# Optimization experiments

Measured on AMD Instinct MI355X. Metric: run time of the kernel, lower is better.

Reference implementation:

```python
import jax, jax.numpy as jnp
import numpy as np
import math

B, C_IN, H, W_DIM, D_DIM = 2, 128, 24, 24, 24
D_MODEL, N_HEAD, N_LAYERS, D_FF = 256, 8, 4, 512
D_K = D_MODEL // N_HEAD
EPS = 1e-6


def setup_inputs() -> dict:
    key = jax.random.key(0)
    ks = jax.random.split(key, 16)
    s = 0.02
    inp = {
        "x": jax.random.normal(ks[0], (B, C_IN, H, W_DIM, D_DIM), jnp.float32),
        # 1x1x1 Conv3d W_x: weight [out, in], bias [out]
        "Wx_w": jax.random.normal(ks[1], (D_MODEL, C_IN), jnp.float32) * s,
        "Wx_b": jnp.zeros((D_MODEL,), jnp.float32),
        # per-layer attention projections (stacked over layers)
        "Wq": jax.random.normal(ks[2], (N_LAYERS, D_MODEL, D_MODEL), jnp.float32) * s,
        "bq": jnp.zeros((N_LAYERS, D_MODEL), jnp.float32),
        "Wk": jax.random.normal(ks[3], (N_LAYERS, D_MODEL, D_MODEL), jnp.float32) * s,
        "bk": jnp.zeros((N_LAYERS, D_MODEL), jnp.float32),
        "Wv": jax.random.normal(ks[4], (N_LAYERS, D_MODEL, D_MODEL), jnp.float32) * s,
        "bv": jnp.zeros((N_LAYERS, D_MODEL), jnp.float32),
        "Wo": jax.random.normal(ks[5], (N_LAYERS, D_MODEL, D_MODEL), jnp.float32) * s,
        "bo": jnp.zeros((N_LAYERS, D_MODEL), jnp.float32),
        # layer norms
        "ln1_g": jnp.ones((N_LAYERS, D_MODEL), jnp.float32),
        "ln1_b": jnp.zeros((N_LAYERS, D_MODEL), jnp.float32),
        "ln2_g": jnp.ones((N_LAYERS, D_MODEL), jnp.float32),
        "ln2_b": jnp.zeros((N_LAYERS, D_MODEL), jnp.float32),
        # FFN
        "ffn_w1": jax.random.normal(ks[6], (N_LAYERS, D_MODEL, D_FF), jnp.float32) * s,
        "ffn_b1": jnp.zeros((N_LAYERS, D_FF), jnp.float32),
        "ffn_w2": jax.random.normal(ks[7], (N_LAYERS, D_FF, D_MODEL), jnp.float32) * s,
        "ffn_b2": jnp.zeros((N_LAYERS, D_MODEL), jnp.float32),
        # depthwise 3x3x3 conv positional encoder (groups = D_MODEL)
        "pos_w": jax.random.normal(ks[8], (N_LAYERS, D_MODEL, 1, 3, 3, 3), jnp.float32) * s,
        "pos_b": jnp.zeros((N_LAYERS, D_MODEL), jnp.float32),
    }
    return inp


def _layer_norm(t, g, b):
    mu = jnp.mean(t, axis=-1, keepdims=True)
    var = jnp.var(t, axis=-1, keepdims=True)
    return (t - mu) * jax.lax.rsqrt(var + EPS) * g + b


def reference(x, Wx_w, Wx_b, Wq, bq, Wk, bk, Wv, bv, Wo, bo,
              ln1_g, ln1_b, ln2_g, ln2_b,
              ffn_w1, ffn_b1, ffn_w2, ffn_b2, pos_w, pos_b):
    b = x.shape[0]
    # 1x1x1 conv projection W_x + ReLU (is_up=False path)
    x = jnp.einsum('bchwd,oc->bohwd', x, Wx_w) + Wx_b[None, :, None, None, None]
    x = jax.nn.relu(x)

    inv_sqrt_dk = 1.0 / math.sqrt(D_K)

    for i in range(N_LAYERS):
        # flatten spatial -> tokens: [b, n, d_model]
        t = jnp.transpose(x.reshape(b, D_MODEL, -1), (0, 2, 1))
        n = t.shape[1]

        def heads(y):  # [b,n,d] -> [b,h,n,dk]
            return jnp.transpose(y.reshape(b, n, N_HEAD, D_K), (0, 2, 1, 3))

        q = heads(t @ Wq[i] + bq[i])
        k = heads(t @ Wk[i] + bk[i])
        v = heads(t @ Wv[i] + bv[i])

        # linear attention: softmax over feature dim for q, token dim for k
        q = jax.nn.softmax(q, axis=-1) * inv_sqrt_dk
        k = jax.nn.softmax(k, axis=-2)
        ctx = jnp.einsum('bhnd,bhne->bhde', k, v)     # [b,h,dk,dk]
        o = jnp.einsum('bhnd,bhde->bhne', q, ctx)      # [b,h,n,dk]
        o = jnp.transpose(o, (0, 2, 1, 3)).reshape(b, n, D_MODEL)
        o = o @ Wo[i] + bo[i]

        t = _layer_norm(t + o, ln1_g[i], ln1_b[i])
        f = jax.nn.gelu(t @ ffn_w1[i] + ffn_b1[i], approximate=False) @ ffn_w2[i] + ffn_b2[i]
        t = _layer_norm(t + f, ln2_g[i], ln2_b[i])

        # back to volume and depthwise conv positional embedding
        x = jnp.transpose(t, (0, 2, 1)).reshape(b, D_MODEL, H, W_DIM, D_DIM)
        pos = jax.lax.conv_general_dilated(
            x, pos_w[i], window_strides=(1, 1, 1), padding='SAME',
            dimension_numbers=('NCDHW', 'OIDHW', 'NCDHW'),
            feature_group_count=D_MODEL,
        ) + pos_b[i][None, :, None, None, None]
        x = x + pos
    return x
```

## Files before the change

kernel.cpp:

```cpp
#include <hip/hip_runtime.h>
#include <math.h>

#define NTOK 13824
#define MTOT 27648
#define BATCH 2
#define CIN 128
#define DMODEL 256
#define NHEAD 8
#define NLAYERS 4
#define DFF 512
#define NSPLIT 27
#define KVHALF ((size_t)BATCH * 256 * NTOK)

typedef float f32x4 __attribute__((ext_vector_type(4)));
typedef __bf16 bf16x8 __attribute__((ext_vector_type(8)));
typedef __attribute__((address_space(1))) void gvoid;
typedef __attribute__((address_space(3))) void lvoid;

#define GLDS16(g, l) __builtin_amdgcn_global_load_lds((gvoid*)(g), (lvoid*)(l), 16, 0, 0)

__device__ __forceinline__ unsigned short f2bf(float f) {
    unsigned u = __float_as_uint(f);
    return (unsigned short)((u + 0x7FFFu + ((u >> 16) & 1u)) >> 16);
}
__device__ __forceinline__ float bf2f(unsigned short h) {
    return __uint_as_float(((unsigned)h) << 16);
}

template<int ACT, int OUTM>
__global__ __launch_bounds__(256) void gemm_bf16(
    const unsigned short* __restrict__ A, int lda,
    const unsigned short* __restrict__ Bt, int ldb,
    const float* __restrict__ bias,
    float* __restrict__ Cf, unsigned short* __restrict__ Cb,
    int ldc, int K, long sA, long sB, long sC)
{
    A  += (size_t)blockIdx.z * sA;
    Bt += (size_t)blockIdx.z * sB;
    if (OUTM == 2) Cf += (size_t)blockIdx.z * sC;
    Cb += (size_t)blockIdx.z * sC;

    __shared__ __attribute__((aligned(16))) unsigned short As[4096];
    __shared__ __attribute__((aligned(16))) unsigned short Bs[4096];
    const int t    = threadIdx.x;
    const int lane = t & 63;
    const int wave = t >> 6;
    const int wm = wave & 1, wn = wave >> 1;
    const int m0 = blockIdx.x * 128, n0 = blockIdx.y * 128;

    const int r0   = t >> 2;
    const int koff = (t & 3) * 8;
    const unsigned short* ga0 = A  + (size_t)(m0 + r0)      * lda + koff;
    const unsigned short* ga1 = A  + (size_t)(m0 + r0 + 64) * lda + koff;
    const unsigned short* gb0 = Bt + (size_t)(n0 + r0)      * ldb + koff;
    const unsigned short* gb1 = Bt + (size_t)(n0 + r0 + 64) * ldb + koff;
    unsigned short* la0 = As + t * 8;
    unsigned short* la1 = As + t * 8 + 2048;
    unsigned short* lb0 = Bs + t * 8;
    unsigned short* lb1 = Bs + t * 8 + 2048;

    f32x4 acc[4][4];
    #pragma unroll
    for (int i = 0; i < 4; ++i)
        #pragma unroll
        for (int j = 0; j < 4; ++j) acc[i][j] = (f32x4)0.0f;

    const int fm = lane & 15;
    const int fq = (lane >> 4) * 8;
    const int arow = (wm * 64 + fm) * 32 + fq;
    const int brow = (wn * 64 + fm) * 32 + fq;

    for (int k0 = 0; k0 < K; k0 += 32) {
        GLDS16(ga0 + k0, la0);
        GLDS16(ga1 + k0, la1);
        GLDS16(gb0 + k0, lb0);
        GLDS16(gb1 + k0, lb1);
        __syncthreads();
        bf16x8 af[4], bg[4];
        #pragma unroll
        for (int i = 0; i < 4; ++i) af[i] = *(const bf16x8*)(As + arow + i * 512);
        #pragma unroll
        for (int j = 0; j < 4; ++j) bg[j] = *(const bf16x8*)(Bs + brow + j * 512);
        #pragma unroll
        for (int i = 0; i < 4; ++i)
            #pragma unroll
            for (int j = 0; j < 4; ++j)
                acc[i][j] = __builtin_amdgcn_mfma_f32_16x16x32_bf16(
                    af[i], bg[j], acc[i][j], 0, 0, 0);
        __syncthreads();
    }

    const int cb  = n0 + wn * 64 + fm;
    const int rbs = m0 + wm * 64 + (lane >> 4) * 4;
    #pragma unroll
    for (int j = 0; j < 4; ++j) {
        const int n = cb + j * 16;
        const float bv = bias[n];
        #pragma unroll
        for (int i = 0; i < 4; ++i) {
            #pragma unroll
            for (int r = 0; r < 4; ++r) {
                float v = acc[i][j][r] + bv;
                if (ACT == 1) v = fmaxf(v, 0.0f);
                if (ACT == 2) v = 0.5f * v * (1.0f + erff(v * 0.7071067811865476f));
                const size_t off = (size_t)(rbs + i * 16 + r) * ldc + n;
                if (OUTM == 2) Cf[off] = v;
                Cb[off] = f2bf(v);
            }
        }
    }
}

#define CW_QKV  786432
#define CW_O   1048576
#define CW_1   1572864
#define CW_2   2097152
#define CW_X   2129920
#define CW_B   2132992
__global__ __launch_bounds__(256) void conv_weights(
    const float* __restrict__ Wq, const float* __restrict__ Wk,
    const float* __restrict__ Wv, const float* __restrict__ Wo,
    const float* __restrict__ fw1, const float* __restrict__ fw2,
    const float* __restrict__ Wx_w,
    const float* __restrict__ bq, const float* __restrict__ bk,
    const float* __restrict__ bv,
    unsigned short* __restrict__ wqkv_t, unsigned short* __restrict__ wo_t,
    unsigned short* __restrict__ w1_t, unsigned short* __restrict__ w2_t,
    unsigned short* __restrict__ wx_bf, float* __restrict__ bqkv)
{
    const int e = blockIdx.x * 256 + threadIdx.x;
    if (e < CW_QKV) {
        const int i = e / 196608, r = e % 196608;
        const int n = r / 256, k = r % 256;
        const float* src = (n < 256) ? Wq : (n < 512) ? Wk : Wv;
        wqkv_t[e] = f2bf(src[((size_t)i * 256 + k) * 256 + (n & 255)]);
    } else if (e < CW_O) {
        const int r = e - CW_QKV;
        const int i = r / 65536, rr = r % 65536, n = rr / 256, k = rr % 256;
        wo_t[r] = f2bf(Wo[((size_t)i * 256 + k) * 256 + n]);
    } else if (e < CW_1) {
        const int r = e - CW_O;
        const int i = r / 131072, rr = r % 131072, n = rr / 256, k = rr % 256;
        w1_t[r] = f2bf(fw1[((size_t)i * 256 + k) * 512 + n]);
    } else if (e < CW_2) {
        const int r = e - CW_1;
        const int i = r / 131072, rr = r % 131072, n = rr / 512, k = rr % 512;
        w2_t[r] = f2bf(fw2[((size_t)i * 512 + k) * 256 + n]);
    } else if (e < CW_X) {
        const int r = e - CW_2;
        wx_bf[r] = f2bf(Wx_w[r]);
    } else if (e < CW_B) {
        const int r = e - CW_X;
        const int i = r / 768, j = r % 768;
        const float v = (j < 256) ? bq[i * 256 + j]
                      : (j < 512) ? bk[i * 256 + j - 256]
                                  : bv[i * 256 + j - 512];
        bqkv[r] = v;
    }
}

__global__ __launch_bounds__(256) void conv_x(
    const float* __restrict__ x, unsigned short* __restrict__ xbf)
{
    __shared__ float tile[32][33];
    const int n0 = blockIdx.x * 32;
    const int c0 = blockIdx.y * 32;
    const int b  = blockIdx.z;
    const int t = threadIdx.x;
    const int tn = t & 31, tc = t >> 5;
    #pragma unroll
    for (int p = 0; p < 4; ++p)
        tile[tc + p * 8][tn] =
            x[((size_t)(b * CIN + c0 + tc + p * 8)) * NTOK + n0 + tn];
    __syncthreads();
    const int cc = t & 31, nr = t >> 5;
    #pragma unroll
    for (int p = 0; p < 4; ++p)
        xbf[((size_t)(b * NTOK + n0 + nr + p * 8)) * CIN + c0 + cc] =
            f2bf(tile[cc][nr + p * 8]);
}

__global__ __launch_bounds__(256) void qsm_kernel(unsigned short* __restrict__ qkv)
{
    const int g = blockIdx.x * 256 + threadIdx.x;
    const int row = g >> 5;
    const int cg  = g & 31;
    unsigned short* p = qkv + (size_t)row * 768 + cg * 8;
    uint4 raw = *(const uint4*)p;
    unsigned short* rp = (unsigned short*)&raw;
    float v[8];
    #pragma unroll
    for (int j = 0; j < 8; ++j) v[j] = bf2f(rp[j]);
    float m = v[0];
    #pragma unroll
    for (int j = 1; j < 8; ++j) m = fmaxf(m, v[j]);
    m = fmaxf(m, __shfl_xor(m, 1, 64));
    m = fmaxf(m, __shfl_xor(m, 2, 64));
    float s = 0.0f;
    #pragma unroll
    for (int j = 0; j < 8; ++j) { v[j] = __expf(v[j] - m); s += v[j]; }
    s += __shfl_xor(s, 1, 64);
    s += __shfl_xor(s, 2, 64);
    const float r = 1.0f / s;
    #pragma unroll
    for (int j = 0; j < 8; ++j) rp[j] = f2bf(v[j] * r);
    *(uint4*)p = raw;
}

__global__ __launch_bounds__(256) void kvt_kernel(
    const unsigned short* __restrict__ qkv, unsigned short* __restrict__ kvT)
{
    const int nb = blockIdx.x, h = blockIdx.y, b = blockIdx.z;
    const int n0 = nb * 64;
    const int t = threadIdx.x;
    __shared__ __attribute__((aligned(16))) unsigned short LT[64 * 72];
    const int tl = t >> 2, cg = t & 3;
    const unsigned short* src =
        qkv + ((size_t)(b * NTOK + n0 + tl)) * 768 + 256 + h * 32 + cg * 8;
    const uint4 kr = *(const uint4*)src;
    const uint4 vr = *(const uint4*)(src + 256);
    const unsigned short* ks = (const unsigned short*)&kr;
    const unsigned short* vs = (const unsigned short*)&vr;
    #pragma unroll
    for (int j = 0; j < 8; ++j) {
        const int ch = cg * 8 + j;
        LT[ch * 72 + tl]        = f2bf(__expf(bf2f(ks[j])));
        LT[(32 + ch) * 72 + tl] = vs[j];
    }
    __syncthreads();
    #pragma unroll
    for (int it = 0; it < 2; ++it) {
        const int idx = it * 256 + t;
        const int row = idx >> 3, seg = idx & 7;
        const uint4 val = *(const uint4*)(LT + row * 72 + seg * 8);
        const int ch = row & 31;
        const size_t dst = ((row >= 32) ? KVHALF : (size_t)0)
                         + ((size_t)(b * 256 + h * 32 + ch)) * NTOK + n0 + seg * 8;
        *(uint4*)(kvT + dst) = val;
    }
}

__global__ __launch_bounds__(256) void ctx_mfma(
    const unsigned short* __restrict__ kvT,
    float* __restrict__ ctxp, float* __restrict__ skp)
{
    const int s = blockIdx.x, h = blockIdx.y, b = blockIdx.z;
    const int t = threadIdx.x, w = t >> 6, l = t & 63;
    const int fm = l & 15, fq = (l >> 4) * 8;
    const size_t rowA = (size_t)(b * 256 + h * 32 + fm) * NTOK;
    const int n0 = s * 512 + w * 128 + fq;
    const unsigned short* pa = kvT + rowA + n0;
    const unsigned short* pb = kvT + KVHALF + rowA + n0;

    f32x4 acc[2][2];
    #pragma unroll
    for (int x = 0; x < 2; ++x)
        #pragma unroll
        for (int y = 0; y < 2; ++y) acc[x][y] = (f32x4)0.0f;
    float ss0 = 0.0f, ss1 = 0.0f;

    #pragma unroll
    for (int step = 0; step < 4; ++step) {
        const int ko = step * 32;
        const uint4 ra0 = *(const uint4*)(pa + ko);
        const uint4 ra1 = *(const uint4*)(pa + (size_t)16 * NTOK + ko);
        const uint4 rb0 = *(const uint4*)(pb + ko);
        const uint4 rb1 = *(const uint4*)(pb + (size_t)16 * NTOK + ko);
        const bf16x8 a0 = *(const bf16x8*)&ra0;
        const bf16x8 a1 = *(const bf16x8*)&ra1;
        const bf16x8 b0 = *(const bf16x8*)&rb0;
        const bf16x8 b1 = *(const bf16x8*)&rb1;
        acc[0][0] = __builtin_amdgcn_mfma_f32_16x16x32_bf16(a0, b0, acc[0][0], 0, 0, 0);
        acc[0][1] = __builtin_amdgcn_mfma_f32_16x16x32_bf16(a0, b1, acc[0][1], 0, 0, 0);
        acc[1][0] = __builtin_amdgcn_mfma_f32_16x16x32_bf16(a1, b0, acc[1][0], 0, 0, 0);
        acc[1][1] = __builtin_amdgcn_mfma_f32_16x16x32_bf16(a1, b1, acc[1][1], 0, 0, 0);
        const unsigned short* u0 = (const unsigned short*)&ra0;
        const unsigned short* u1 = (const unsigned short*)&ra1;
        #pragma unroll
        for (int j = 0; j < 8; ++j) { ss0 += bf2f(u0[j]); ss1 += bf2f(u1[j]); }
    }

    ss0 += __shfl_xor(ss0, 16, 64); ss0 += __shfl_xor(ss0, 32, 64);
    ss1 += __shfl_xor(ss1, 16, 64); ss1 += __shfl_xor(ss1, 32, 64);
    __shared__ float skw[4][32];
    __shared__ float redc[4][32][33];
    if (l < 16) { skw[w][fm] = ss0; skw[w][16 + fm] = ss1; }

    const int rb4 = (l >> 4) * 4;
    #pragma unroll
    for (int x = 0; x < 2; ++x)
        #pragma unroll
        for (int y = 0; y < 2; ++y)
            #pragma unroll
            for (int r = 0; r < 4; ++r)
                redc[w][x * 16 + rb4 + r][y * 16 + fm] = acc[x][y][r];
    __syncthreads();

    if (t < 32)
        skp[(size_t)s * 512 + b * 256 + h * 32 + t] =
            skw[0][t] + skw[1][t] + skw[2][t] + skw[3][t];

    const int e0 = t * 4;
    const int dd = e0 >> 5, c0 = e0 & 31;
    float4 o;
    o.x = redc[0][dd][c0+0] + redc[1][dd][c0+0] + redc[2][dd][c0+0] + redc[3][dd][c0+0];
    o.y = redc[0][dd][c0+1] + redc[1][dd][c0+1] + redc[2][dd][c0+1] + redc[3][dd][c0+1];
    o.z = redc[0][dd][c0+2] + redc[1][dd][c0+2] + redc[2][dd][c0+2] + redc[3][dd][c0+2];
    o.w = redc[0][dd][c0+3] + redc[1][dd][c0+3] + redc[2][dd][c0+3] + redc[3][dd][c0+3];
    *(float4*)(ctxp + ((size_t)s * 16 + b * 8 + h) * 1024 + e0) = o;
}

__global__ __launch_bounds__(256) void ctxred(
    const float* __restrict__ ctxp, const float* __restrict__ skp,
    float* __restrict__ ctx, float* __restrict__ Sk)
{
    const int o = blockIdx.x * 256 + threadIdx.x;
    if (o < 16384) {
        float a = 0.0f;
        for (int s = 0; s < NSPLIT; ++s) a += ctxp[(size_t)s * 16384 + o];
        ctx[o] = a;
    } else {
        const int c = o - 16384;
        float a = 0.0f;
        for (int s = 0; s < NSPLIT; ++s) a += skp[(size_t)s * 512 + c];
        Sk[c] = a;
    }
}

__global__ __launch_bounds__(256) void ctxwo_kernel(
    const float* __restrict__ ctx, const float* __restrict__ Sk,
    const unsigned short* __restrict__ wo_t, unsigned short* __restrict__ wp)
{
    const int h = blockIdx.x, b = blockIdx.y;
    const int n = threadIdx.x;
    __shared__ float cl[1024];
    __shared__ float sdk[32];
    {
        const float* cp = ctx + (size_t)(b * 8 + h) * 1024;
        *(float4*)&cl[n * 4] = *(const float4*)&cp[n * 4];
    }
    if (n < 32) sdk[n] = 0.17677669529663687f / Sk[b * 256 + h * 32 + n];
    __syncthreads();
    float w[32];
    const unsigned short* wop = wo_t + (size_t)n * 256 + h * 32;
    #pragma unroll
    for (int e = 0; e < 32; ++e) w[e] = bf2f(wop[e]);
    unsigned short outv[32];
    #pragma unroll
    for (int d = 0; d < 32; ++d) {
        float acc = 0.0f;
        #pragma unroll
        for (int e = 0; e < 32; ++e) acc += cl[d * 32 + e] * w[e];
        outv[d] = f2bf(acc * sdk[d]);
    }
    unsigned short* op = wp + (size_t)b * 65536 + (size_t)n * 256 + h * 32;
    #pragma unroll
    for (int d = 0; d < 32; d += 8)
        *(uint4*)(op + d) = *(uint4*)(outv + d);
}

template<int WB>
__global__ __launch_bounds__(256) void ln_kernel(
    float* __restrict__ t, const unsigned short* __restrict__ add,
    const float* __restrict__ g, const float* __restrict__ bta,
    unsigned short* __restrict__ tbf)
{
    const int row = blockIdx.x;
    const int c = threadIdx.x;
    const int lane = c & 63, wave = c >> 6;
    const size_t off = (size_t)row * 256 + c;
    const float v = t[off] + bf2f(add[off]);
    __shared__ float red[8];
    float s = v;
    #pragma unroll
    for (int o = 32; o; o >>= 1) s += __shfl_xor(s, o, 64);
    if (lane == 0) red[wave] = s;
    __syncthreads();
    const float mu = (red[0] + red[1] + red[2] + red[3]) * (1.0f / 256.0f);
    const float dv = v - mu;
    float s2 = dv * dv;
    #pragma unroll
    for (int o = 32; o; o >>= 1) s2 += __shfl_xor(s2, o, 64);
    if (lane == 0) red[wave + 4] = s2;
    __syncthreads();
    const float var = (red[4] + red[5] + red[6] + red[7]) * (1.0f / 256.0f);
    const float o = dv * rsqrtf(var + 1e-6f) * g[c] + bta[c];
    t[off] = o;
    if (WB) tbf[off] = f2bf(o);
}

template<int WB>
__global__ __launch_bounds__(256) void posconv_kernel(
    const float* __restrict__ tin, const float* __restrict__ pw,
    const float* __restrict__ pb, float* __restrict__ outp,
    unsigned short* __restrict__ tbfp)
{
    const int hw = blockIdx.x;
    const int b  = blockIdx.y;
    const int hh = hw / 24, ww = hw % 24;
    const int c  = threadIdx.x;

    float w[27];
    #pragma unroll
    for (int k = 0; k < 27; ++k) w[k] = pw[c * 27 + k];
    const float bias = pb[c];

    const float* base = tin + (size_t)b * NTOK * 256 + c;

    const float* colp[9];
    bool colok[9];
    #pragma unroll
    for (int dh = -1; dh <= 1; ++dh)
        #pragma unroll
        for (int dw = -1; dw <= 1; ++dw) {
            const int j = (dh + 1) * 3 + (dw + 1);
            const int h2 = hh + dh, w2 = ww + dw;
            colok[j] = ((unsigned)h2 < 24u) & ((unsigned)w2 < 24u);
            colp[j] = base + (size_t)((h2 * 24 + w2) * 24) * 256;
        }

    float win[9][3];
    #pragma unroll
    for (int j = 0; j < 9; ++j) {
        win[j][0] = 0.0f;
        win[j][1] = colok[j] ? colp[j][0] : 0.0f;
    }

    float* ob = outp + ((size_t)b * NTOK + (size_t)hw * 24) * 256 + c;
    unsigned short* tb = WB ? (tbfp + ((size_t)b * NTOK + (size_t)hw * 24) * 256 + c)
                            : (unsigned short*)nullptr;

    for (int d = 0; d < 24; ++d) {
        #pragma unroll
        for (int j = 0; j < 9; ++j)
            win[j][2] = (colok[j] && d < 23) ? colp[j][(d + 1) * 256] : 0.0f;

        float acc = bias + win[4][1];
        #pragma unroll
        for (int j = 0; j < 9; ++j) {
            acc += w[j * 3 + 0] * win[j][0];
            acc += w[j * 3 + 1] * win[j][1];
            acc += w[j * 3 + 2] * win[j][2];
        }
        ob[d * 256] = acc;
        if (WB) tb[d * 256] = f2bf(acc);

        #pragma unroll
        for (int j = 0; j < 9; ++j) { win[j][0] = win[j][1]; win[j][1] = win[j][2]; }
    }
}

__global__ __launch_bounds__(256) void tr_out(
    const float* __restrict__ tin, float* __restrict__ outp)
{
    __shared__ float tile[32][33];
    const int m0 = blockIdx.x * 32;
    const int c0 = blockIdx.y * 32;
    const int t = threadIdx.x;
    const int tc = t & 31, tr = t >> 5;
    #pragma unroll
    for (int r = 0; r < 4; ++r)
        tile[tr + r * 8][tc] = tin[(size_t)(m0 + tr + r * 8) * 256 + c0 + tc];
    __syncthreads();
    const int b = (m0 >= NTOK) ? 1 : 0;
    const int n0 = m0 - b * NTOK;
    #pragma unroll
    for (int r = 0; r < 4; ++r)
        outp[((size_t)b * 256 + c0 + tr + r * 8) * NTOK + n0 + tc] = tile[tc][tr + r * 8];
}

extern "C" void kernel_launch(void* const* d_in, const int* in_sizes, int n_in,
                              void* d_out, int out_size, void* d_ws, size_t ws_size,
                              hipStream_t stream)
{
    (void)in_sizes; (void)n_in; (void)out_size; (void)ws_size;
    const float* x     = (const float*)d_in[0];
    const float* Wx_w  = (const float*)d_in[1];
    const float* Wx_b  = (const float*)d_in[2];
    const float* Wq    = (const float*)d_in[3];
    const float* bq    = (const float*)d_in[4];
    const float* Wk    = (const float*)d_in[5];
    const float* bk    = (const float*)d_in[6];
    const float* Wv    = (const float*)d_in[7];
    const float* bv    = (const float*)d_in[8];
    const float* Wo    = (const float*)d_in[9];
    const float* bo    = (const float*)d_in[10];
    const float* ln1_g = (const float*)d_in[11];
    const float* ln1_b = (const float*)d_in[12];
    const float* ln2_g = (const float*)d_in[13];
    const float* ln2_b = (const float*)d_in[14];
    const float* fw1   = (const float*)d_in[15];
    const float* fb1   = (const float*)d_in[16];
    const float* fw2   = (const float*)d_in[17];
    const float* fb2   = (const float*)d_in[18];
    const float* pw    = (const float*)d_in[19];
    const float* pb    = (const float*)d_in[20];
    float* out = (float*)d_out;

    char* p = (char*)d_ws;
    float* tA            = (float*)p;          p += (size_t)MTOT * 256 * 4;
    float* tB            = (float*)p;          p += (size_t)MTOT * 256 * 4;
    unsigned short* tbf  = (unsigned short*)p; p += (size_t)MTOT * 256 * 2;
    unsigned short* qkv  = (unsigned short*)p; p += (size_t)MTOT * 768 * 2;
    unsigned short* hbf  = (unsigned short*)p; p += (size_t)MTOT * 512 * 2;
    unsigned short* ob   = (unsigned short*)p; p += (size_t)MTOT * 256 * 2;
    unsigned short* xbf  = (unsigned short*)p; p += (size_t)MTOT * 128 * 2;
    unsigned short* wqkv_t = (unsigned short*)p; p += (size_t)786432 * 2;
    unsigned short* wo_t   = (unsigned short*)p; p += (size_t)262144 * 2;
    unsigned short* w1_t   = (unsigned short*)p; p += (size_t)524288 * 2;
    unsigned short* w2_t   = (unsigned short*)p; p += (size_t)524288 * 2;
    unsigned short* wx_bf  = (unsigned short*)p; p += (size_t)32768 * 2;
    unsigned short* wp     = (unsigned short*)p; p += (size_t)BATCH * 65536 * 2;
    float* bqkv = (float*)p; p += 3072 * 4;
    float* ctx  = (float*)p; p += 16384 * 4;
    float* Sk   = (float*)p; p += 512 * 4;
    float* ctxp = (float*)p; p += (size_t)NSPLIT * 16384 * 4;
    float* skp  = (float*)p; p += (size_t)NSPLIT * 512 * 4;
    unsigned short* kvT = hbf;

    hipLaunchKernelGGL(conv_weights, dim3(8333), dim3(256), 0, stream,
                       Wq, Wk, Wv, Wo, fw1, fw2, Wx_w, bq, bk, bv,
                       wqkv_t, wo_t, w1_t, w2_t, wx_bf, bqkv);
    hipLaunchKernelGGL(conv_x, dim3(NTOK / 32, CIN / 32, BATCH), dim3(256), 0, stream,
                       x, xbf);

    hipLaunchKernelGGL((gemm_bf16<1, 2>), dim3(216, 2, 1), dim3(256), 0, stream,
                       xbf, CIN, wx_bf, CIN, Wx_b, tA, tbf, 256, CIN,
                       (long)0, (long)0, (long)0);

    for (int i = 0; i < NLAYERS; ++i) {
        float* tin  = (i & 1) ? tB : tA;
        float* tout = (i & 1) ? tA : tB;

        hipLaunchKernelGGL((gemm_bf16<0, 1>), dim3(216, 6, 1), dim3(256), 0, stream,
                           tbf, 256, wqkv_t + (size_t)i * 196608, 256,
                           bqkv + i * 768, nullptr, qkv, 768, 256,
                           (long)0, (long)0, (long)0);

        hipLaunchKernelGGL(kvt_kernel, dim3(NTOK / 64, NHEAD, BATCH), dim3(256), 0, stream,
                           qkv, kvT);
        hipLaunchKernelGGL(ctx_mfma, dim3(NSPLIT, NHEAD, BATCH), dim3(256), 0, stream,
                           kvT, ctxp, skp);
        hipLaunchKernelGGL(ctxred, dim3(66), dim3(256), 0, stream, ctxp, skp, ctx, Sk);

        hipLaunchKernelGGL(qsm_kernel, dim3(3456), dim3(256), 0, stream, qkv);
        hipLaunchKernelGGL(ctxwo_kernel, dim3(NHEAD, BATCH), dim3(256), 0, stream,
                           ctx, Sk, wo_t + (size_t)i * 65536, wp);

        hipLaunchKernelGGL((gemm_bf16<0, 1>), dim3(108, 2, BATCH), dim3(256), 0, stream,
                           qkv, 768, wp, 256, bo + i * 256, nullptr, ob, 256, 256,
                           (long)NTOK * 768, (long)65536, (long)NTOK * 256);

        hipLaunchKernelGGL((ln_kernel<1>), dim3(MTOT), dim3(256), 0, stream,
                           tin, ob, ln1_g + i * 256, ln1_b + i * 256, tbf);

        hipLaunchKernelGGL((gemm_bf16<2, 1>), dim3(216, 4, 1), dim3(256), 0, stream,
                           tbf, 256, w1_t + (size_t)i * 131072, 256,
                           fb1 + i * 512, nullptr, hbf, 512, 256,
                           (long)0, (long)0, (long)0);
        hipLaunchKernelGGL((gemm_bf16<0, 1>), dim3(216, 2, 1), dim3(256), 0, stream,
                           hbf, 512, w2_t + (size_t)i * 131072, 512,
                           fb2 + i * 256, nullptr, ob, 256, 512,
                           (long)0, (long)0, (long)0);
        hipLaunchKernelGGL((ln_kernel<0>), dim3(MTOT), dim3(256), 0, stream,
                           tin, ob, ln2_g + i * 256, ln2_b + i * 256, nullptr);

        if (i < NLAYERS - 1)
            hipLaunchKernelGGL((posconv_kernel<1>), dim3(576, BATCH), dim3(256), 0, stream,
                               tin, pw + (size_t)i * 6912, pb + i * 256, tout, tbf);
        else
            hipLaunchKernelGGL((posconv_kernel<0>), dim3(576, BATCH), dim3(256), 0, stream,
                               tin, pw + (size_t)i * 6912, pb + i * 256, tout, nullptr);
    }

    hipLaunchKernelGGL(tr_out, dim3(MTOT / 32, 8), dim3(256), 0, stream, tA, out);
}
```

Before: 905.0 us.

## Replace LDS-staged GEMM with direct-load MFMA GEMM and fuse q softmax into epilogue

The GEMM no longer stages tiles through LDS with global_load_lds. Each wave now loads its MFMA fragments straight from global memory, which removes the barriers, and K is a compile-time constant so the loop can unroll. MFMA operands are swapped so each lane holds 4 consecutive columns, and the epilogue writes vectorized bias loads and ushort4/float4 stores. The Q projection becomes its own launch whose epilogue applies the per-head feature softmax with cross-lane shuffles, so the separate qsm pass over qkv is dropped. The cost is that tiles are no longer shared through LDS, so every wave re-reads its fragments from global or L2.

```diff
diff --git a/kernel.cpp b/kernel.cpp
--- a/kernel.cpp
+++ b/kernel.cpp
@@ -14,10 +14,6 @@
 
 typedef float f32x4 __attribute__((ext_vector_type(4)));
 typedef __bf16 bf16x8 __attribute__((ext_vector_type(8)));
-typedef __attribute__((address_space(1))) void gvoid;
-typedef __attribute__((address_space(3))) void lvoid;
-
-#define GLDS16(g, l) __builtin_amdgcn_global_load_lds((gvoid*)(g), (lvoid*)(l), 16, 0, 0)
 
 __device__ __forceinline__ unsigned short f2bf(float f) {
     unsigned u = __float_as_uint(f);
@@ -27,37 +23,28 @@
     return __uint_as_float(((unsigned)h) << 16);
 }
 
-template<int ACT, int OUTM>
-__global__ __launch_bounds__(256) void gemm_bf16(
+template<int ACT, int OUTM, int QSM, int KC>
+__global__ __launch_bounds__(256) void gemm_direct(
     const unsigned short* __restrict__ A, int lda,
     const unsigned short* __restrict__ Bt, int ldb,
     const float* __restrict__ bias,
     float* __restrict__ Cf, unsigned short* __restrict__ Cb,
-    int ldc, int K, long sA, long sB, long sC)
+    int ldc, long sA, long sB, long sC)
 {
     A  += (size_t)blockIdx.z * sA;
     Bt += (size_t)blockIdx.z * sB;
     if (OUTM == 2) Cf += (size_t)blockIdx.z * sC;
     Cb += (size_t)blockIdx.z * sC;
 
-    __shared__ __attribute__((aligned(16))) unsigned short As[4096];
-    __shared__ __attribute__((aligned(16))) unsigned short Bs[4096];
-    const int t    = threadIdx.x;
-    const int lane = t & 63;
-    const int wave = t >> 6;
+    const int t = threadIdx.x, lane = t & 63, wave = t >> 6;
     const int wm = wave & 1, wn = wave >> 1;
-    const int m0 = blockIdx.x * 128, n0 = blockIdx.y * 128;
-
-    const int r0   = t >> 2;
-    const int koff = (t & 3) * 8;
-    const unsigned short* ga0 = A  + (size_t)(m0 + r0)      * lda + koff;
-    const unsigned short* ga1 = A  + (size_t)(m0 + r0 + 64) * lda + koff;
-    const unsigned short* gb0 = Bt + (size_t)(n0 + r0)      * ldb + koff;
-    const unsigned short* gb1 = Bt + (size_t)(n0 + r0 + 64) * ldb + koff;
-    unsigned short* la0 = As + t * 8;
-    unsigned short* la1 = As + t * 8 + 2048;
-    unsigned short* lb0 = Bs + t * 8;
-    unsigned short* lb1 = Bs + t * 8 + 2048;
+    const int m0 = blockIdx.x * 128 + wm * 64;
+    const int n0 = blockIdx.y * 128 + wn * 64;
+    const int fm = lane & 15, fq = lane >> 4;
+    const int ko = fq * 8;
+
+    const unsigned short* pa = A  + (size_t)(m0 + fm) * lda + ko;
+    const unsigned short* pb = Bt + (size_t)(n0 + fm) * ldb + ko;
 
     f32x4 acc[4][4];
     #pragma unroll
@@ -65,48 +52,90 @@
         #pragma unroll
         for (int j = 0; j < 4; ++j) acc[i][j] = (f32x4)0.0f;
 
-    const int fm = lane & 15;
-    const int fq = (lane >> 4) * 8;
-    const int arow = (wm * 64 + fm) * 32 + fq;
-    const int brow = (wn * 64 + fm) * 32 + fq;
-
-    for (int k0 = 0; k0 < K; k0 += 32) {
-        GLDS16(ga0 + k0, la0);
-        GLDS16(ga1 + k0, la1);
-        GLDS16(gb0 + k0, lb0);
-        GLDS16(gb1 + k0, lb1);
-        __syncthreads();
+    #pragma unroll 4
+    for (int s = 0; s < KC; ++s) {
+        const int k0 = s * 32;
         bf16x8 af[4], bg[4];
         #pragma unroll
-        for (int i = 0; i < 4; ++i) af[i] = *(const bf16x8*)(As + arow + i * 512);
-        #pragma unroll
-        for (int j = 0; j < 4; ++j) bg[j] = *(const bf16x8*)(Bs + brow + j * 512);
+        for (int i = 0; i < 4; ++i) {
+            const uint4 r4 = *(const uint4*)(pa + (size_t)i * 16 * lda + k0);
+            af[i] = *(const bf16x8*)&r4;
+        }
+        #pragma unroll
+        for (int j = 0; j < 4; ++j) {
+            const uint4 r4 = *(const uint4*)(pb + (size_t)j * 16 * ldb + k0);
+            bg[j] = *(const bf16x8*)&r4;
+        }
         #pragma unroll
         for (int i = 0; i < 4; ++i)
             #pragma unroll
             for (int j = 0; j < 4; ++j)
                 acc[i][j] = __builtin_amdgcn_mfma_f32_16x16x32_bf16(
-                    af[i], bg[j], acc[i][j], 0, 0, 0);
-        __syncthreads();
-    }
-
-    const int cb  = n0 + wn * 64 + fm;
-    const int rbs = m0 + wm * 64 + (lane >> 4) * 4;
-    #pragma unroll
-    for (int j = 0; j < 4; ++j) {
-        const int n = cb + j * 16;
-        const float bv = bias[n];
-        #pragma unroll
-        for (int i = 0; i < 4; ++i) {
+                    bg[j], af[i], acc[i][j], 0, 0, 0);
+    }
+
+    const int fq4 = fq * 4;
+    #pragma unroll
+    for (int i = 0; i < 4; ++i) {
+        const int m = m0 + i * 16 + fm;
+        float v[4][4];
+        #pragma unroll
+        for (int j = 0; j < 4; ++j) {
+            const float4 b4 = *(const float4*)(bias + n0 + j * 16 + fq4);
+            v[j][0] = acc[i][j][0] + b4.x;
+            v[j][1] = acc[i][j][1] + b4.y;
+            v[j][2] = acc[i][j][2] + b4.z;
+            v[j][3] = acc[i][j][3] + b4.w;
+            if (ACT == 1) {
+                #pragma unroll
+                for (int r = 0; r < 4; ++r) v[j][r] = fmaxf(v[j][r], 0.0f);
+            }
+            if (ACT == 2) {
+                #pragma unroll
+                for (int r = 0; r < 4; ++r)
+                    v[j][r] = 0.5f * v[j][r] *
+                              (1.0f + erff(v[j][r] * 0.7071067811865476f));
+            }
+        }
+        if (QSM) {
             #pragma unroll
-            for (int r = 0; r < 4; ++r) {
-                float v = acc[i][j][r] + bv;
-                if (ACT == 1) v = fmaxf(v, 0.0f);
-                if (ACT == 2) v = 0.5f * v * (1.0f + erff(v * 0.7071067811865476f));
-                const size_t off = (size_t)(rbs + i * 16 + r) * ldc + n;
-                if (OUTM == 2) Cf[off] = v;
-                Cb[off] = f2bf(v);
+            for (int g = 0; g < 2; ++g) {
+                float mx = -1e30f;
+                #pragma unroll
+                for (int j = 2 * g; j < 2 * g + 2; ++j)
+                    #pragma unroll
+                    for (int r = 0; r < 4; ++r) mx = fmaxf(mx, v[j][r]);
+                mx = fmaxf(mx, __shfl_xor(mx, 16, 64));
+                mx = fmaxf(mx, __shfl_xor(mx, 32, 64));
+                float s = 0.0f;
+                #pragma unroll
+                for (int j = 2 * g; j < 2 * g + 2; ++j)
+                    #pragma unroll
+                    for (int r = 0; r < 4; ++r) {
+                        v[j][r] = __expf(v[j][r] - mx);
+                        s += v[j][r];
+                    }
+                s += __shfl_xor(s, 16, 64);
+                s += __shfl_xor(s, 32, 64);
+                const float rs = 1.0f / s;
+                #pragma unroll
+                for (int j = 2 * g; j < 2 * g + 2; ++j)
+                    #pragma unroll
+                    for (int r = 0; r < 4; ++r) v[j][r] *= rs;
             }
+        }
+        #pragma unroll
+        for (int j = 0; j < 4; ++j) {
+            const size_t off = (size_t)m * ldc + n0 + j * 16 + fq4;
+            if (OUTM == 2) {
+                float4 o4;
+                o4.x = v[j][0]; o4.y = v[j][1]; o4.z = v[j][2]; o4.w = v[j][3];
+                *(float4*)(Cf + off) = o4;
+            }
+            ushort4 u4;
+            u4.x = f2bf(v[j][0]); u4.y = f2bf(v[j][1]);
+            u4.z = f2bf(v[j][2]); u4.w = f2bf(v[j][3]);
+            *(ushort4*)(Cb + off) = u4;
         }
     }
 }
@@ -180,33 +209,6 @@
             f2bf(tile[cc][nr + p * 8]);
 }
 
-__global__ __launch_bounds__(256) void qsm_kernel(unsigned short* __restrict__ qkv)
-{
-    const int g = blockIdx.x * 256 + threadIdx.x;
-    const int row = g >> 5;
-    const int cg  = g & 31;
-    unsigned short* p = qkv + (size_t)row * 768 + cg * 8;
-    uint4 raw = *(const uint4*)p;
-    unsigned short* rp = (unsigned short*)&raw;
-    float v[8];
-    #pragma unroll
-    for (int j = 0; j < 8; ++j) v[j] = bf2f(rp[j]);
-    float m = v[0];
-    #pragma unroll
-    for (int j = 1; j < 8; ++j) m = fmaxf(m, v[j]);
-    m = fmaxf(m, __shfl_xor(m, 1, 64));
-    m = fmaxf(m, __shfl_xor(m, 2, 64));
-    float s = 0.0f;
-    #pragma unroll
-    for (int j = 0; j < 8; ++j) { v[j] = __expf(v[j] - m); s += v[j]; }
-    s += __shfl_xor(s, 1, 64);
-    s += __shfl_xor(s, 2, 64);
-    const float r = 1.0f / s;
-    #pragma unroll
-    for (int j = 0; j < 8; ++j) rp[j] = f2bf(v[j] * r);
-    *(uint4*)p = raw;
-}
-
 __global__ __launch_bounds__(256) void kvt_kernel(
     const unsigned short* __restrict__ qkv, unsigned short* __restrict__ kvT)
 {
@@ -524,17 +526,21 @@
     hipLaunchKernelGGL(conv_x, dim3(NTOK / 32, CIN / 32, BATCH), dim3(256), 0, stream,
                        x, xbf);
 
-    hipLaunchKernelGGL((gemm_bf16<1, 2>), dim3(216, 2, 1), dim3(256), 0, stream,
-                       xbf, CIN, wx_bf, CIN, Wx_b, tA, tbf, 256, CIN,
+    hipLaunchKernelGGL((gemm_direct<1, 2, 0, 4>), dim3(216, 2, 1), dim3(256), 0, stream,
+                       xbf, CIN, wx_bf, CIN, Wx_b, tA, tbf, 256,
                        (long)0, (long)0, (long)0);
 
     for (int i = 0; i < NLAYERS; ++i) {
         float* tin  = (i & 1) ? tB : tA;
         float* tout = (i & 1) ? tA : tB;
 
-        hipLaunchKernelGGL((gemm_bf16<0, 1>), dim3(216, 6, 1), dim3(256), 0, stream,
+        hipLaunchKernelGGL((gemm_direct<0, 1, 1, 8>), dim3(216, 2, 1), dim3(256), 0, stream,
                            tbf, 256, wqkv_t + (size_t)i * 196608, 256,
-                           bqkv + i * 768, nullptr, qkv, 768, 256,
+                           bqkv + i * 768, nullptr, qkv, 768,
+                           (long)0, (long)0, (long)0);
+        hipLaunchKernelGGL((gemm_direct<0, 1, 0, 8>), dim3(216, 4, 1), dim3(256), 0, stream,
+                           tbf, 256, wqkv_t + (size_t)i * 196608 + 65536, 256,
+                           bqkv + i * 768 + 256, nullptr, qkv + 256, 768,
                            (long)0, (long)0, (long)0);
 
         hipLaunchKernelGGL(kvt_kernel, dim3(NTOK / 64, NHEAD, BATCH), dim3(256), 0, stream,
@@ -543,24 +549,23 @@
                            kvT, ctxp, skp);
         hipLaunchKernelGGL(ctxred, dim3(66), dim3(256), 0, stream, ctxp, skp, ctx, Sk);
 
-        hipLaunchKernelGGL(qsm_kernel, dim3(3456), dim3(256), 0, stream, qkv);
         hipLaunchKernelGGL(ctxwo_kernel, dim3(NHEAD, BATCH), dim3(256), 0, stream,
                            ctx, Sk, wo_t + (size_t)i * 65536, wp);
 
-        hipLaunchKernelGGL((gemm_bf16<0, 1>), dim3(108, 2, BATCH), dim3(256), 0, stream,
-                           qkv, 768, wp, 256, bo + i * 256, nullptr, ob, 256, 256,
+        hipLaunchKernelGGL((gemm_direct<0, 1, 0, 8>), dim3(108, 2, BATCH), dim3(256), 0, stream,
+                           qkv, 768, wp, 256, bo + i * 256, nullptr, ob, 256,
                            (long)NTOK * 768, (long)65536, (long)NTOK * 256);
 
         hipLaunchKernelGGL((ln_kernel<1>), dim3(MTOT), dim3(256), 0, stream,
                            tin, ob, ln1_g + i * 256, ln1_b + i * 256, tbf);
 
-        hipLaunchKernelGGL((gemm_bf16<2, 1>), dim3(216, 4, 1), dim3(256), 0, stream,
+        hipLaunchKernelGGL((gemm_direct<2, 1, 0, 8>), dim3(216, 4, 1), dim3(256), 0, stream,
                            tbf, 256, w1_t + (size_t)i * 131072, 256,
-                           fb1 + i * 512, nullptr, hbf, 512, 256,
+                           fb1 + i * 512, nullptr, hbf, 512,
                            (long)0, (long)0, (long)0);
-        hipLaunchKernelGGL((gemm_bf16<0, 1>), dim3(216, 2, 1), dim3(256), 0, stream,
+        hipLaunchKernelGGL((gemm_direct<0, 1, 0, 16>), dim3(216, 2, 1), dim3(256), 0, stream,
                            hbf, 512, w2_t + (size_t)i * 131072, 512,
-                           fb2 + i * 256, nullptr, ob, 256, 512,
+                           fb2 + i * 256, nullptr, ob, 256,
                            (long)0, (long)0, (long)0);
         hipLaunchKernelGGL((ln_kernel<0>), dim3(MTOT), dim3(256), 0, stream,
                            tin, ob, ln2_g + i * 256, ln2_b + i * 256, nullptr);
```

New measurement: 1.340 ms. +48.1%, slower.
